# Kernel tuning notes

Measured on AMD Instinct MI355X. Metric: run time of the kernel, lower is better.

## Reference

```python
import jax, jax.numpy as jnp
import numpy as np

H = 16        # num_attention_heads
D = 1024      # hidden_size
HD = D // H   # head_dim = 64


def setup_inputs() -> dict:
    key = jax.random.key(0)
    ks = jax.random.split(key, 5)
    B, T = 16, 1024
    s_in = 1.0 / np.sqrt(D)
    return {
        "hidden_states": jax.random.normal(ks[0], (B, T, D), dtype=jnp.float32),
        "w_qkv": jax.random.normal(ks[1], (D, 3 * D), dtype=jnp.float32) * s_in,
        "b_qkv": jnp.zeros((3 * D,), dtype=jnp.float32),
        "w_out": jax.random.normal(ks[2], (D, D), dtype=jnp.float32) * s_in,
        "b_out": jnp.zeros((D,), dtype=jnp.float32),
    }


def reference(hidden_states, w_qkv, b_qkv, w_out, b_out):
    B, T, C = hidden_states.shape
    qkv = hidden_states @ w_qkv + b_qkv                      # [B,T,3C]
    q, k, v = jnp.split(qkv, 3, axis=-1)
    # [B,T,C] -> [B,H,T,HD]
    q = q.reshape(B, T, H, HD).transpose(0, 2, 1, 3)
    k = k.reshape(B, T, H, HD).transpose(0, 2, 1, 3)
    v = v.reshape(B, T, H, HD).transpose(0, 2, 1, 3)
    scale = 1.0 / np.sqrt(HD)
    logits = jnp.einsum("bhqd,bhkd->bhqk", q, k) * scale     # [B,H,T,T]
    attn = jax.nn.softmax(logits, axis=-1)
    out = jnp.einsum("bhqk,bhkd->bhqd", attn, v)             # [B,H,T,HD]
    out = out.transpose(0, 2, 1, 3).reshape(B, T, C)
    return out @ w_out + b_out
```

## Files before the change

### kernel.cpp

```cpp
#include <hip/hip_runtime.h>
#include <cstdint>
#include <cstddef>

typedef _Float16 h8 __attribute__((ext_vector_type(8)));
typedef _Float16 h4 __attribute__((ext_vector_type(4)));
typedef __fp16 fp16x2 __attribute__((ext_vector_type(2)));
typedef float f4 __attribute__((ext_vector_type(4)));

#define MFMA(a, b, c) __builtin_amdgcn_mfma_f32_16x16x32_f16((a), (b), (c), 0, 0, 0)

__device__ __forceinline__ void gl_lds16(const void* g, void* l) {
  __builtin_amdgcn_global_load_lds((const __attribute__((address_space(1))) void*)g,
                                   (__attribute__((address_space(3))) void*)l, 16, 0, 0);
}

__device__ __forceinline__ h8 lds_frag(const char* base, int r, int ch) {
  return *(const h8*)(base + ((r * 8 + (ch ^ (r & 7))) * 16));
}

__device__ __forceinline__ void BAR() {
  asm volatile("" ::: "memory");
  __builtin_amdgcn_s_barrier();
  asm volatile("" ::: "memory");
}

__global__ void k_cvt_hs(const float* __restrict__ in, _Float16* __restrict__ out, int n8) {
  int i = blockIdx.x * blockDim.x + threadIdx.x;
  if (i >= n8) return;
  size_t idx = (size_t)i * 8;
  float4 a = *(const float4*)(in + idx);
  float4 b = *(const float4*)(in + idx + 4);
  h8 o;
  o[0] = (_Float16)a.x; o[1] = (_Float16)a.y; o[2] = (_Float16)a.z; o[3] = (_Float16)a.w;
  o[4] = (_Float16)b.x; o[5] = (_Float16)b.y; o[6] = (_Float16)b.z; o[7] = (_Float16)b.w;
  *(h8*)(out + idx) = o;
}

__global__ void k_transcvt(const float* __restrict__ in, _Float16* __restrict__ out, int N, int K) {
  __shared__ float tile[64 * 65];
  int tn = blockIdx.x * 64, tk = blockIdx.y * 64;
  for (int i = 0; i < 4; ++i) {
    int cid = i * 256 + threadIdx.x;
    int r = cid >> 4, c4 = cid & 15;
    float4 v = *(const float4*)(in + (size_t)(tk + r) * N + tn + c4 * 4);
    tile[r * 65 + c4 * 4 + 0] = v.x; tile[r * 65 + c4 * 4 + 1] = v.y;
    tile[r * 65 + c4 * 4 + 2] = v.z; tile[r * 65 + c4 * 4 + 3] = v.w;
  }
  __syncthreads();
  for (int i = 0; i < 2; ++i) {
    int cid = i * 256 + threadIdx.x;
    int n = cid >> 3, kc = cid & 7;
    h8 o;
    for (int j = 0; j < 8; ++j) o[j] = (_Float16)tile[(kc * 8 + j) * 65 + n];
    *(h8*)(out + (size_t)(tn + n) * K + tk + kc * 8) = o;
  }
}

__device__ __forceinline__ void gemm256_tile(
    const _Float16* __restrict__ Ab, const _Float16* __restrict__ Bb,
    const _Float16* __restrict__ BbN, bool first, bool more,
    char* smem, f4 (&acc)[8][4]) {
  constexpr int TILE = 32768, HALF = 16384;
  int tid = threadIdx.x, lane = tid & 63, wave = tid >> 6;
  int l15 = lane & 15, l4 = lane >> 4;
  int wm = (wave >> 2) * 128, wn = (wave & 3) * 64;
  int rs = tid >> 3, cg = (tid & 7) ^ (rs & 7);
  char* cA = smem;            char* nA = smem + TILE;
  char* cB = smem + 2 * TILE; char* nB = smem + 3 * TILE;

  auto stA = [&](int kt, int h, char* dst) {
    const _Float16* s = Ab + (size_t)(h * 128 + rs) * 1024 + kt + cg * 8;
    gl_lds16(s, dst + h * HALF + tid * 16);
    gl_lds16(s + (size_t)64 * 1024, dst + h * HALF + 8192 + tid * 16);
  };
  auto stB = [&](const _Float16* base, int kt, int h, char* dst) {
    const _Float16* s = base + (size_t)(h * 128 + rs) * 1024 + kt + cg * 8;
    gl_lds16(s, dst + h * HALF + tid * 16);
    gl_lds16(s + (size_t)64 * 1024, dst + h * HALF + 8192 + tid * 16);
  };

  if (first) {
    stA(0, 0, cA); stA(0, 1, cA);
    stB(Bb, 0, 0, cB); stB(Bb, 0, 1, cB);
    stB(Bb, 64, 0, nB); stB(Bb, 64, 1, nB);
    asm volatile("s_waitcnt vmcnt(4)" ::: "memory");
    BAR();
  }

  h8 af[4][2], bf[4][2];
  for (int u = 0; u < 16; ++u) {
    int kt1 = (u + 1) << 6, kt2 = (u + 2) << 6;
#pragma unroll
    for (int mi = 0; mi < 4; ++mi) {
      int r = wm + mi * 16 + l15;
      af[mi][0] = lds_frag(cA, r, l4);
      af[mi][1] = lds_frag(cA, r, 4 + l4);
    }
#pragma unroll
    for (int nj = 0; nj < 2; ++nj) {
      int r = wn + nj * 16 + l15;
      bf[nj][0] = lds_frag(cB, r, l4);
      bf[nj][1] = lds_frag(cB, r, 4 + l4);
    }
    if (u < 15) stA(kt1, 0, nA);
    else if (more) stA(0, 0, nA);
    asm volatile("s_waitcnt lgkmcnt(8)" ::: "memory");
    BAR();
    asm volatile("s_waitcnt lgkmcnt(0)" ::: "memory");
    __builtin_amdgcn_s_setprio(1);
#pragma unroll
    for (int kk = 0; kk < 2; ++kk)
#pragma unroll
      for (int mi = 0; mi < 4; ++mi)
#pragma unroll
        for (int nj = 0; nj < 2; ++nj)
          acc[mi][nj] = MFMA(af[mi][kk], bf[nj][kk], acc[mi][nj]);
    __builtin_amdgcn_s_setprio(0);
    BAR();
#pragma unroll
    for (int nj = 2; nj < 4; ++nj) {
      int r = wn + nj * 16 + l15;
      bf[nj][0] = lds_frag(cB, r, l4);
      bf[nj][1] = lds_frag(cB, r, 4 + l4);
    }
    if (u < 15) stA(kt1, 1, nA);
    else if (more) stA(0, 1, nA);
    BAR();
    asm volatile("s_waitcnt lgkmcnt(0)" ::: "memory");
    __builtin_amdgcn_s_setprio(1);
#pragma unroll
    for (int kk = 0; kk < 2; ++kk)
#pragma unroll
      for (int mi = 0; mi < 4; ++mi)
#pragma unroll
        for (int nj = 2; nj < 4; ++nj)
          acc[mi][nj] = MFMA(af[mi][kk], bf[nj][kk], acc[mi][nj]);
    __builtin_amdgcn_s_setprio(0);
    BAR();
#pragma unroll
    for (int mi = 0; mi < 4; ++mi) {
      int r = wm + 64 + mi * 16 + l15;
      af[mi][0] = lds_frag(cA, r, l4);
      af[mi][1] = lds_frag(cA, r, 4 + l4);
    }
    if (u < 14) stB(Bb, kt2, 0, cB);
    else if (more) stB(BbN, (u == 14) ? 0 : 64, 0, cB);
    BAR();
    asm volatile("s_waitcnt lgkmcnt(0)" ::: "memory");
    __builtin_amdgcn_s_setprio(1);
#pragma unroll
    for (int kk = 0; kk < 2; ++kk)
#pragma unroll
      for (int mi = 0; mi < 4; ++mi)
#pragma unroll
        for (int nj = 2; nj < 4; ++nj)
          acc[4 + mi][nj] = MFMA(af[mi][kk], bf[nj][kk], acc[4 + mi][nj]);
    __builtin_amdgcn_s_setprio(0);
    BAR();
    if (u < 14) stB(Bb, kt2, 1, cB);
    else if (more) stB(BbN, (u == 14) ? 0 : 64, 1, cB);
    if (u < 14 || more) asm volatile("s_waitcnt vmcnt(4)" ::: "memory");
    else                asm volatile("s_waitcnt vmcnt(0)" ::: "memory");
    BAR();
    __builtin_amdgcn_s_setprio(1);
#pragma unroll
    for (int kk = 0; kk < 2; ++kk)
#pragma unroll
      for (int mi = 0; mi < 4; ++mi)
#pragma unroll
        for (int nj = 0; nj < 2; ++nj)
          acc[4 + mi][nj] = MFMA(af[mi][kk], bf[nj][kk], acc[4 + mi][nj]);
    __builtin_amdgcn_s_setprio(0);
    BAR();
    char* t = cA; cA = nA; nA = t;
    t = cB; cB = nB; nB = t;
  }
}

__global__ __launch_bounds__(512) void k_gemm_qkv(
    const _Float16* __restrict__ A, const _Float16* __restrict__ BT,
    const float* __restrict__ bias,
    _Float16* __restrict__ Q, _Float16* __restrict__ Kq, _Float16* __restrict__ Vt) {
  __shared__ char smem[131072];
  int id = blockIdx.x;
  int swz = (id & 7) * 32 + (id >> 3);
  int by = swz >> 2, c = swz & 3;
  int tm = by * 256;
  const _Float16* Ab = A + (size_t)tm * 1024;
  int tid = threadIdx.x, lane = tid & 63, wave = tid >> 6;
  int l15 = lane & 15, l4 = lane >> 4;
  int wm = (wave >> 2) * 128, wn = (wave & 3) * 64;

  for (int t = 0; t < 3; ++t) {
    int tn = (t * 4 + c) * 256;
    const _Float16* Bb = BT + (size_t)tn * 1024;
    const _Float16* BbN = Bb + (size_t)1024 * 1024;
    f4 acc[8][4] = {};
    gemm256_tile(Ab, Bb, BbN, t == 0, t < 2, smem, acc);

    if (t < 2) {
      _Float16* dst = (t == 0) ? Q : Kq;
#pragma unroll
      for (int nj = 0; nj < 4; ++nj) {
        int n = tn + wn + nj * 16 + l15;
        float bv = bias[n];
        int h = (n >> 6) & 15, d = n & 63;
#pragma unroll
        for (int mig = 0; mig < 8; ++mig) {
#pragma unroll
          for (int r = 0; r < 4; ++r) {
            int m = tm + wm + mig * 16 + l4 * 4 + r;
            int b = m >> 10, tt = m & 1023;
            dst[(((size_t)b * 16 + h) * 1024 + tt) * 64 + d] =
                (_Float16)(acc[mig][nj][r] + bv);
          }
        }
      }
    } else {
      _Float16* L = (_Float16*)smem;
      int b = tm >> 10, tb = tm & 1023;
#pragma unroll
      for (int p = 0; p < 2; ++p) {
        __syncthreads();
        if (((wave >> 1) & 1) == p) {
          int nloc = (wave & 1) * 64;
#pragma unroll
          for (int nj = 0; nj < 4; ++nj) {
            int nl = nloc + nj * 16 + l15;
            float bv = bias[tn + p * 128 + nl];
#pragma unroll
            for (int mig = 0; mig < 8; ++mig) {
              h4 pk;
#pragma unroll
              for (int r = 0; r < 4; ++r) pk[r] = (_Float16)(acc[mig][nj][r] + bv);
              *(h4*)(L + nl * 264 + wm + mig * 16 + l4 * 4) = pk;
            }
          }
        }
        __syncthreads();
#pragma unroll
        for (int i = 0; i < 8; ++i) {
          int cid = i * 512 + tid;
          int nl = cid >> 5, tc = cid & 31;
          int ng = tn + p * 128 + nl;
          int h = (ng >> 6) & 15, d = ng & 63;
          *(h8*)(Vt + (((size_t)b * 16 + h) * 64 + d) * 1024 + tb + tc * 8) =
              *(const h8*)(L + nl * 264 + tc * 8);
        }
      }
    }
  }
}

__global__ __launch_bounds__(256, 2) void k_attn(
    const _Float16* __restrict__ Q, const _Float16* __restrict__ Kk,
    const _Float16* __restrict__ Vt, _Float16* __restrict__ O) {
  __shared__ char smem[20480 + 32768];
  _Float16* sP = (_Float16*)smem;
  char* sKV = smem + 20480;
  const float SCL = 0.125f * 1.44269504088896340736f;
  int tid = threadIdx.x, wave = tid >> 6, lane = tid & 63;
  int l15 = lane & 15, l4 = lane >> 4;
  int bh = blockIdx.y;
  int qt = blockIdx.x * 256;
  const _Float16* Qb = Q + (size_t)bh * 65536;
  const _Float16* Kb = Kk + (size_t)bh * 65536;
  const _Float16* Vb = Vt + (size_t)bh * 65536;

  h8 qf[4][2];
#pragma unroll
  for (int nt = 0; nt < 4; ++nt) {
    int r = qt + wave * 64 + nt * 16 + l15;
#pragma unroll
    for (int kk = 0; kk < 2; ++kk)
      qf[nt][kk] = *(const h8*)(Qb + (size_t)r * 64 + (kk * 4 + l4) * 8);
  }
  _Float16 scl_h = (_Float16)SCL;
#pragma unroll
  for (int nt = 0; nt < 4; ++nt)
#pragma unroll
    for (int kk = 0; kk < 2; ++kk)
#pragma unroll
      for (int j = 0; j < 8; ++j) qf[nt][kk][j] *= scl_h;

  int cid0 = tid, cid1 = tid + 256;
  int r0 = cid0 >> 3, c0 = (cid0 & 7) ^ (r0 & 7);
  int r1 = cid1 >> 3, c1 = (cid1 & 7) ^ (r1 & 7);
  const _Float16* kp0 = Kb + (size_t)r0 * 64 + c0 * 8;
  const _Float16* kp1 = Kb + (size_t)r1 * 64 + c1 * 8;
  const _Float16* vp0 = Vb + (size_t)r0 * 1024 + c0 * 8;
  const _Float16* vp1 = Vb + (size_t)r1 * 1024 + c1 * 8;

  auto stage = [&](int it, int b) {
    char* dK = sKV + b * 16384;
    char* dV = dK + 8192;
    size_t ko = (size_t)it * 4096;
    size_t vo = (size_t)it * 64;
    gl_lds16(kp0 + ko, dK + cid0 * 16);
    gl_lds16(kp1 + ko, dK + cid1 * 16);
    gl_lds16(vp0 + vo, dV + cid0 * 16);
    gl_lds16(vp1 + vo, dV + cid1 * 16);
  };

  f4 oacc[4][4] = {};
  f4 lacc[4] = {};
  h8 ones;
#pragma unroll
  for (int j = 0; j < 8; ++j) ones[j] = (_Float16)1.0f;
  _Float16* pw = sP + wave * 64 * 40;

  stage(0, 0);
  asm volatile("s_waitcnt vmcnt(0)" ::: "memory");
  BAR();

  for (int it = 0; it < 16; ++it) {
    int cur = it & 1;
    if (it < 15) stage(it + 1, cur ^ 1);
    const char* sK = sKV + cur * 16384;
    const char* sV = sK + 8192;
    for (int mh = 0; mh < 2; ++mh) {
      f4 sacc[2][4] = {};
#pragma unroll
      for (int kk = 0; kk < 2; ++kk) {
        h8 kf[2];
        int ch = kk * 4 + l4;
#pragma unroll
        for (int mt = 0; mt < 2; ++mt) {
          int r = mh * 32 + mt * 16 + l15;
          kf[mt] = *(const h8*)(sK + ((r * 8 + (ch ^ (r & 7))) * 16));
        }
#pragma unroll
        for (int mt = 0; mt < 2; ++mt)
#pragma unroll
          for (int nt = 0; nt < 4; ++nt)
            sacc[mt][nt] = MFMA(kf[mt], qf[nt][kk], sacc[mt][nt]);
      }
#pragma unroll
      for (int mt = 0; mt < 2; ++mt) {
#pragma unroll
        for (int nt = 0; nt < 4; ++nt) {
          float p0 = __builtin_amdgcn_exp2f(sacc[mt][nt][0]);
          float p1 = __builtin_amdgcn_exp2f(sacc[mt][nt][1]);
          float p2 = __builtin_amdgcn_exp2f(sacc[mt][nt][2]);
          float p3 = __builtin_amdgcn_exp2f(sacc[mt][nt][3]);
          union { fp16x2 h[2]; h4 v; } uu;
          uu.h[0] = __builtin_amdgcn_cvt_pkrtz(p0, p1);
          uu.h[1] = __builtin_amdgcn_cvt_pkrtz(p2, p3);
          *(h4*)(pw + (nt * 16 + l15) * 40 + mt * 16 + l4 * 4) = uu.v;
        }
      }
      h8 pf[4], vf[4];
#pragma unroll
      for (int mi = 0; mi < 4; ++mi)
        pf[mi] = *(const h8*)(pw + (mi * 16 + l15) * 40 + l4 * 8);
      int ch = mh * 4 + l4;
#pragma unroll
      for (int nd = 0; nd < 4; ++nd) {
        int r = nd * 16 + l15;
        vf[nd] = *(const h8*)(sV + ((r * 8 + (ch ^ (r & 7))) * 16));
      }
#pragma unroll
      for (int mi = 0; mi < 4; ++mi) {
#pragma unroll
        for (int nd = 0; nd < 4; ++nd)
          oacc[mi][nd] = MFMA(pf[mi], vf[nd], oacc[mi][nd]);
        lacc[mi] = MFMA(pf[mi], ones, lacc[mi]);
      }
    }
    asm volatile("s_waitcnt vmcnt(0)" ::: "memory");
    BAR();
  }
  int b = bh >> 4, h = bh & 15;
#pragma unroll
  for (int mi = 0; mi < 4; ++mi) {
#pragma unroll
    for (int r = 0; r < 4; ++r) {
      float inv = 1.f / lacc[mi][r];
      int t = qt + wave * 64 + mi * 16 + l4 * 4 + r;
#pragma unroll
      for (int nd = 0; nd < 4; ++nd)
        O[(size_t)(b * 1024 + t) * 1024 + h * 64 + nd * 16 + l15] =
            (_Float16)(oacc[mi][nd][r] * inv);
    }
  }
}

__global__ __launch_bounds__(512) void k_gemm_out(
    const _Float16* __restrict__ A, const _Float16* __restrict__ BT,
    const float* __restrict__ bias, float* __restrict__ C) {
  __shared__ char smem[131072];
  int id = blockIdx.x;
  int swz = (id & 7) * 32 + (id >> 3);
  int by = swz >> 2, bx = swz & 3;
  int tm = by * 256, tn = bx * 256;
  f4 acc[8][4] = {};
  gemm256_tile(A + (size_t)tm * 1024, BT + (size_t)tn * 1024, nullptr,
               true, false, smem, acc);

  int tid = threadIdx.x, lane = tid & 63, wave = tid >> 6;
  int l15 = lane & 15, l4 = lane >> 4;
  int wm = (wave >> 2) * 128, wn = (wave & 3) * 64;
#pragma unroll
  for (int nj = 0; nj < 4; ++nj) {
    int n = tn + wn + nj * 16 + l15;
    float bv = bias[n];
#pragma unroll
    for (int mig = 0; mig < 8; ++mig) {
#pragma unroll
      for (int r = 0; r < 4; ++r) {
        int m = tm + wm + mig * 16 + l4 * 4 + r;
        C[(size_t)m * 1024 + n] = acc[mig][nj][r] + bv;
      }
    }
  }
}

extern "C" void kernel_launch(void* const* d_in, const int* in_sizes, int n_in,
                              void* d_out, int out_size, void* d_ws, size_t ws_size,
                              hipStream_t stream) {
  const float* hs    = (const float*)d_in[0];
  const float* w_qkv = (const float*)d_in[1];
  const float* b_qkv = (const float*)d_in[2];
  const float* w_out = (const float*)d_in[3];
  const float* b_out = (const float*)d_in[4];
  float* out = (float*)d_out;
  char* ws = (char*)d_ws;

  _Float16* hs_h  = (_Float16*)(ws);
  _Float16* wqkvT = (_Float16*)(ws + 33554432);
  _Float16* woutT = (_Float16*)(ws + 39845888);
  _Float16* q_ws  = (_Float16*)(ws + 41943040);
  _Float16* k_ws  = (_Float16*)(ws + 75497472);
  _Float16* vt_ws = (_Float16*)(ws + 109051904);

  k_cvt_hs<<<8192, 256, 0, stream>>>(hs, hs_h, 2097152);
  k_transcvt<<<dim3(48, 16), 256, 0, stream>>>(w_qkv, wqkvT, 3072, 1024);
  k_transcvt<<<dim3(16, 16), 256, 0, stream>>>(w_out, woutT, 1024, 1024);
  k_gemm_qkv<<<256, 512, 0, stream>>>(hs_h, wqkvT, b_qkv, q_ws, k_ws, vt_ws);
  _Float16* attn_h = hs_h;
  k_attn<<<dim3(4, 256), 256, 0, stream>>>(q_ws, k_ws, vt_ws, attn_h);
  k_gemm_out<<<256, 512, 0, stream>>>(attn_h, woutT, b_out, out);
}
```

Before: 359.2 us.

## Merge preprocessing kernels and triple-buffer K/V staging in attention

Merges the hidden-state conversion and both weight transpose-conversions into one launch, which removes two kernel launches and their gaps. The attention kernel grows its K/V LDS ring from two to three buffers and prefetches two iterations ahead, using a partial vmcnt wait so global loads overlap more compute. The final normalization swaps the division for a hardware reciprocal. Extra LDS per block (about 69KB) could limit occupancy at two blocks per CU, and rcp carries slightly lower precision.

```diff
diff --git a/kernel.cpp b/kernel.cpp
--- a/kernel.cpp
+++ b/kernel.cpp
@@ -24,21 +24,26 @@
   asm volatile("" ::: "memory");
 }
 
-__global__ void k_cvt_hs(const float* __restrict__ in, _Float16* __restrict__ out, int n8) {
-  int i = blockIdx.x * blockDim.x + threadIdx.x;
-  if (i >= n8) return;
-  size_t idx = (size_t)i * 8;
-  float4 a = *(const float4*)(in + idx);
-  float4 b = *(const float4*)(in + idx + 4);
-  h8 o;
-  o[0] = (_Float16)a.x; o[1] = (_Float16)a.y; o[2] = (_Float16)a.z; o[3] = (_Float16)a.w;
-  o[4] = (_Float16)b.x; o[5] = (_Float16)b.y; o[6] = (_Float16)b.z; o[7] = (_Float16)b.w;
-  *(h8*)(out + idx) = o;
-}
-
-__global__ void k_transcvt(const float* __restrict__ in, _Float16* __restrict__ out, int N, int K) {
+__global__ void k_pre(const float* __restrict__ hs, _Float16* __restrict__ hs_h,
+                      const float* __restrict__ w_qkv, _Float16* __restrict__ wqkvT,
+                      const float* __restrict__ w_out, _Float16* __restrict__ woutT) {
+  int id = blockIdx.x;
+  if (id < 8192) {
+    size_t idx = ((size_t)id * 256 + threadIdx.x) * 8;
+    float4 a = *(const float4*)(hs + idx);
+    float4 b = *(const float4*)(hs + idx + 4);
+    h8 o;
+    o[0] = (_Float16)a.x; o[1] = (_Float16)a.y; o[2] = (_Float16)a.z; o[3] = (_Float16)a.w;
+    o[4] = (_Float16)b.x; o[5] = (_Float16)b.y; o[6] = (_Float16)b.z; o[7] = (_Float16)b.w;
+    *(h8*)(hs_h + idx) = o;
+    return;
+  }
   __shared__ float tile[64 * 65];
-  int tn = blockIdx.x * 64, tk = blockIdx.y * 64;
+  const float* in; _Float16* out; int N, bx, by;
+  if (id < 8960) { int t = id - 8192; in = w_qkv; out = wqkvT; N = 3072; bx = t % 48; by = t / 48; }
+  else           { int t = id - 8960; in = w_out; out = woutT; N = 1024; bx = t & 15; by = t >> 4; }
+  const int K = 1024;
+  int tn = bx * 64, tk = by * 64;
   for (int i = 0; i < 4; ++i) {
     int cid = i * 256 + threadIdx.x;
     int r = cid >> 4, c4 = cid & 15;
@@ -255,7 +260,7 @@
 __global__ __launch_bounds__(256, 2) void k_attn(
     const _Float16* __restrict__ Q, const _Float16* __restrict__ Kk,
     const _Float16* __restrict__ Vt, _Float16* __restrict__ O) {
-  __shared__ char smem[20480 + 32768];
+  __shared__ char smem[20480 + 49152];
   _Float16* sP = (_Float16*)smem;
   char* sKV = smem + 20480;
   const float SCL = 0.125f * 1.44269504088896340736f;
@@ -309,13 +314,13 @@
   for (int j = 0; j < 8; ++j) ones[j] = (_Float16)1.0f;
   _Float16* pw = sP + wave * 64 * 40;
 
-  stage(0, 0);
-  asm volatile("s_waitcnt vmcnt(0)" ::: "memory");
+  stage(0, 0); stage(1, 1);
+  asm volatile("s_waitcnt vmcnt(4)" ::: "memory");
   BAR();
 
+  int cur = 0, nb = 2;
   for (int it = 0; it < 16; ++it) {
-    int cur = it & 1;
-    if (it < 15) stage(it + 1, cur ^ 1);
+    if (it < 14) stage(it + 2, nb);
     const char* sK = sKV + cur * 16384;
     const char* sV = sK + 8192;
     for (int mh = 0; mh < 2; ++mh) {
@@ -367,15 +372,18 @@
         lacc[mi] = MFMA(pf[mi], ones, lacc[mi]);
       }
     }
-    asm volatile("s_waitcnt vmcnt(0)" ::: "memory");
-    BAR();
+    if (it < 14) asm volatile("s_waitcnt vmcnt(4)" ::: "memory");
+    else         asm volatile("s_waitcnt vmcnt(0)" ::: "memory");
+    BAR();
+    cur = (cur == 2) ? 0 : cur + 1;
+    nb = (nb == 2) ? 0 : nb + 1;
   }
   int b = bh >> 4, h = bh & 15;
 #pragma unroll
   for (int mi = 0; mi < 4; ++mi) {
 #pragma unroll
     for (int r = 0; r < 4; ++r) {
-      float inv = 1.f / lacc[mi][r];
+      float inv = __builtin_amdgcn_rcpf(lacc[mi][r]);
       int t = qt + wave * 64 + mi * 16 + l4 * 4 + r;
 #pragma unroll
       for (int nd = 0; nd < 4; ++nd)
@@ -433,9 +441,7 @@
   _Float16* k_ws  = (_Float16*)(ws + 75497472);
   _Float16* vt_ws = (_Float16*)(ws + 109051904);
 
-  k_cvt_hs<<<8192, 256, 0, stream>>>(hs, hs_h, 2097152);
-  k_transcvt<<<dim3(48, 16), 256, 0, stream>>>(w_qkv, wqkvT, 3072, 1024);
-  k_transcvt<<<dim3(16, 16), 256, 0, stream>>>(w_out, woutT, 1024, 1024);
+  k_pre<<<9216, 256, 0, stream>>>(hs, hs_h, w_qkv, wqkvT, w_out, woutT);
   k_gemm_qkv<<<256, 512, 0, stream>>>(hs_h, wqkvT, b_qkv, q_ws, k_ws, vt_ws);
   _Float16* attn_h = hs_h;
   k_attn<<<dim3(4, 256), 256, 0, stream>>>(q_ws, k_ws, vt_ws, attn_h);
```

New measurement: 358.4 us. About the same (-0.2%).
